# Performance work log

Hardware: AMD Instinct MI355X
Metric: run time of the kernel (lower is better)

Reference implementation:

```python
import jax, jax.numpy as jnp
import numpy as np

PALACE_N = 64   # base palace mask size
PALACE_BLOCK = 8  # 8 palaces of 8 positions each


def _palace_base():
    # base 64x64 mask: 1.0 within a palace (8x8 diagonal blocks), 0.5 across palaces
    pid = jnp.arange(PALACE_N) // PALACE_BLOCK
    intra = pid[:, None] == pid[None, :]
    return jnp.where(intra, 1.0, 0.5).astype(jnp.float32)


def _get_mask(T, inter_palace_weight):
    # tile base mask by index modulo 64 (matches mask[i % 64, j % 64])
    base = _palace_base()
    ii = jnp.arange(T) % PALACE_N
    base_T = base[ii[:, None], ii[None, :]]            # [T, T]
    intra = (base_T == 1.0).astype(jnp.float32)
    inter = (base_T < 1.0).astype(jnp.float32)
    return intra + jax.nn.sigmoid(inter_palace_weight) * inter


def setup_inputs() -> dict:
    key = jax.random.key(0)
    ks = jax.random.split(key, 5)
    B, T, D = 4, 2048, 1024
    x = jax.random.normal(ks[0], (B, T, D), dtype=jnp.float32)
    s = 1.0 / np.sqrt(D)
    Wq = jax.random.normal(ks[1], (D, D), dtype=jnp.float32) * s
    Wk = jax.random.normal(ks[2], (D, D), dtype=jnp.float32) * s
    Wv = jax.random.normal(ks[3], (D, D), dtype=jnp.float32) * s
    inter_palace_weight = jnp.float32(0.1)
    return {"x": x, "Wq": Wq, "Wk": Wk, "Wv": Wv,
            "inter_palace_weight": inter_palace_weight}


def reference(x, Wq, Wk, Wv, inter_palace_weight):
    B, T, D = x.shape
    H = 16
    hd = D // H
    scale = hd ** -0.5
    pmask = _get_mask(T, inter_palace_weight)          # [T, T]
    # torch Linear: x @ W.T
    q = (x @ Wq.T).reshape(B, T, H, hd)
    k = (x @ Wk.T).reshape(B, T, H, hd)
    v = (x @ Wv.T).reshape(B, T, H, hd)
    attn = jnp.einsum('bqhd,bkhd->bhqk', q, k) * scale
    attn = attn * pmask[None, None, :, :]
    attn = jax.nn.softmax(attn, axis=-1)
    attn = jnp.nan_to_num(attn, nan=0.0)
    out = jnp.einsum('bhqk,bkhd->bqhd', attn, v)
    return out.reshape(B, T, D)
```

## Files before the change

kernel.cpp:

```cpp
#include <hip/hip_runtime.h>

typedef unsigned short u16;
typedef unsigned int u32;
typedef short bf16x8 __attribute__((ext_vector_type(8)));
typedef short bf16x4 __attribute__((ext_vector_type(4)));
typedef float f32x4 __attribute__((ext_vector_type(4)));
typedef u32 u32x2 __attribute__((ext_vector_type(2)));

#define AS_GLOBAL __attribute__((address_space(1)))
#define AS_LDS __attribute__((address_space(3)))

#if defined(__HIP_DEVICE_COMPILE__)
#define MFMA16(a, b, c) __builtin_amdgcn_mfma_f32_16x16x16bf16_1k(a, b, c, 0, 0, 0)
#else
#define MFMA16(a, b, c) (c)
#endif

__device__ __forceinline__ void async16(const void* g, void* l) {
  __builtin_amdgcn_global_load_lds((const AS_GLOBAL u32*)g, (AS_LDS u32*)l, 16, 0, 0);
}

__device__ __forceinline__ u16 f2bf(float f) {
  u32 u = __builtin_bit_cast(u32, f);
  u += 0x7FFFu + ((u >> 16) & 1u);
  return (u16)(u >> 16);
}

__device__ __forceinline__ u32 pk2bf(float lo, float hi) {
  return __builtin_amdgcn_perm(__builtin_bit_cast(u32, hi),
                               __builtin_bit_cast(u32, lo), 0x07060302u);
}

__device__ __forceinline__ float fexp2(float x) {
#if __has_builtin(__builtin_amdgcn_exp2f)
  return __builtin_amdgcn_exp2f(x);
#else
  return exp2f(x);
#endif
}

__global__ __launch_bounds__(256) void cvt_all(const float* __restrict__ x,
                                               const float* __restrict__ wq,
                                               const float* __restrict__ wk,
                                               const float* __restrict__ wv,
                                               u16* __restrict__ xb,
                                               u16* __restrict__ wb) {
  const int blk = blockIdx.x;
  const float* src;
  u16* dst;
  int i;
  if (blk < 8192) {
    src = x; dst = xb; i = blk * 256 + threadIdx.x;
  } else if (blk < 9216) {
    src = wq; dst = wb; i = (blk - 8192) * 256 + threadIdx.x;
  } else if (blk < 10240) {
    src = wk; dst = wb + 1048576; i = (blk - 9216) * 256 + threadIdx.x;
  } else {
    src = wv; dst = wb + 2097152; i = (blk - 10240) * 256 + threadIdx.x;
  }
  float4 f = reinterpret_cast<const float4*>(src)[i];
  ushort4 o;
  o.x = f2bf(f.x); o.y = f2bf(f.y); o.z = f2bf(f.z); o.w = f2bf(f.w);
  reinterpret_cast<ushort4*>(dst)[i] = o;
}

__global__ __launch_bounds__(256, 3) void qkv_gemm(const u16* __restrict__ X,
                                                   const u16* __restrict__ W,
                                                   u16* __restrict__ O) {
  const int z = blockIdx.z;
  const u16* Wz = W + (size_t)z * (1024 * 1024);
  u16* Oz = O + (size_t)z * (8192 * 1024);

  __shared__ __align__(16) u16 As[2][128 * 32];
  __shared__ __align__(16) u16 Bs[2][128 * 32];

  const int t = threadIdx.x;
  const int lane = t & 63, w = t >> 6, quad = lane >> 4, lq = lane & 15;
  const int wm = (w >> 1) * 64, wn = (w & 1) * 64;
  const size_t m0 = (size_t)blockIdx.x * 128;
  const int n0 = blockIdx.y * 128;
  const int srow = t >> 2, sseg = (t & 3) * 8;

  f32x4 acc[4][4];
#pragma unroll
  for (int i = 0; i < 4; ++i)
#pragma unroll
    for (int j = 0; j < 4; ++j) acc[i][j] = f32x4{0.f, 0.f, 0.f, 0.f};

  const u16* ga = X + (m0 + srow) * 1024 + sseg;
  const u16* gb = Wz + (size_t)(n0 + srow) * 1024 + sseg;

  async16(ga, &As[0][srow * 32 + sseg]);
  async16(ga + 64 * 1024, &As[0][(64 + srow) * 32 + sseg]);
  async16(gb, &Bs[0][srow * 32 + sseg]);
  async16(gb + 64 * 1024, &Bs[0][(64 + srow) * 32 + sseg]);

  for (int kt = 0; kt < 32; ++kt) {
    const int cur = kt & 1;
    __syncthreads();
    if (kt < 31) {
      const int k1 = (kt + 1) * 32;
      async16(ga + k1, &As[cur ^ 1][srow * 32 + sseg]);
      async16(ga + 64 * 1024 + k1, &As[cur ^ 1][(64 + srow) * 32 + sseg]);
      async16(gb + k1, &Bs[cur ^ 1][srow * 32 + sseg]);
      async16(gb + 64 * 1024 + k1, &Bs[cur ^ 1][(64 + srow) * 32 + sseg]);
    }
    bf16x8 af[4], bfr[4];
#pragma unroll
    for (int i = 0; i < 4; ++i)
      af[i] = *reinterpret_cast<const bf16x8*>(&As[cur][(wm + i * 16 + lq) * 32 + quad * 8]);
#pragma unroll
    for (int j = 0; j < 4; ++j)
      bfr[j] = *reinterpret_cast<const bf16x8*>(&Bs[cur][(wn + j * 16 + lq) * 32 + quad * 8]);
#pragma unroll
    for (int i = 0; i < 4; ++i)
#pragma unroll
      for (int j = 0; j < 4; ++j)
        acc[i][j] = __builtin_amdgcn_mfma_f32_16x16x32_bf16(af[i], bfr[j], acc[i][j], 0, 0, 0);
  }

#pragma unroll
  for (int i = 0; i < 4; ++i) {
#pragma unroll
    for (int j = 0; j < 4; ++j) {
      const int n = n0 + wn + j * 16 + lq;
      const int hh = n >> 6, d = n & 63;
#pragma unroll
      for (int r = 0; r < 4; ++r) {
        const size_t m = m0 + wm + i * 16 + quad * 4 + r;
        const size_t bb = m >> 11, tt = m & 2047;
        if (z != 2)
          Oz[((bb * 16 + hh) * 2048 + tt) * 64 + d] = f2bf(acc[i][j][r]);
        else
          Oz[((bb * 16 + hh) * 64 + d) * 2048 + tt] = f2bf(acc[i][j][r]);
      }
    }
  }
}

__global__ __launch_bounds__(256, 2) void palace_attn(const u16* __restrict__ Q,
                                                      const u16* __restrict__ K,
                                                      const u16* __restrict__ Vt,
                                                      float* __restrict__ out,
                                                      const float* __restrict__ wptr) {
  const int bh = blockIdx.x, qt = blockIdx.y;
  const int h = bh & 15, b = bh >> 4;
  const size_t base = (size_t)bh * (2048 * 64);

  __shared__ __align__(16) u16 Ks[2][64 * 64];
  __shared__ __align__(16) u16 Vs[2][64 * 64];

  const int t = threadIdx.x;
  const int w = t >> 6, lane = t & 63, quad = lane >> 4, lq = lane & 15;
  const int q1 = quad >> 1, q0 = quad & 1, x7 = lq & 7;
  const float sig = 1.f / (1.f + __expf(-wptr[0]));
  const float Ci = 0.125f * 1.44269504f;
  const float Co = Ci * sig;
  const float MC = 14.4269504f;

  const float Cd = ((lq >> 3) == q1) ? Ci : Co;

  bf16x8 qf[4][2];
#pragma unroll
  for (int qg = 0; qg < 4; ++qg)
#pragma unroll
    for (int kc = 0; kc < 2; ++kc)
      qf[qg][kc] = *reinterpret_cast<const bf16x8*>(
          Q + base + (size_t)(qt * 256 + w * 64 + qg * 16 + lq) * 64 + kc * 32 + quad * 8);

  int ko[2], vo[2];
#pragma unroll
  for (int r = 0; r < 2; ++r) {
    const int slot = r * 256 + t;
    const int row = slot >> 3;
    const int cl = (slot & 7) ^ (row & 7);
    ko[r] = row * 64 + cl * 8;
    vo[r] = row * 2048 + cl * 8;
  }

  f32x4 O[4][4];
  float lsum[4] = {0.f, 0.f, 0.f, 0.f};
#pragma unroll
  for (int qg = 0; qg < 4; ++qg)
#pragma unroll
    for (int dg = 0; dg < 4; ++dg) O[qg][dg] = f32x4{0.f, 0.f, 0.f, 0.f};

  {
    const u16* kgp = K + base;
    const u16* vgp = Vt + base;
    async16(kgp + ko[0], &Ks[0][(w * 64) * 8]);
    async16(kgp + ko[1], &Ks[0][(256 + w * 64) * 8]);
    async16(vgp + vo[0], &Vs[0][(w * 64) * 8]);
    async16(vgp + vo[1], &Vs[0][(256 + w * 64) * 8]);
  }

  for (int kt = 0; kt < 32; ++kt) {
    const int cur = kt & 1;
    __syncthreads();
    if (kt < 31) {
      const u16* kgp = K + base + (size_t)(kt + 1) * 4096;
      const u16* vgp = Vt + base + (size_t)(kt + 1) * 64;
      const int nb = cur ^ 1;
      async16(kgp + ko[0], &Ks[nb][(w * 64) * 8]);
      async16(kgp + ko[1], &Ks[nb][(256 + w * 64) * 8]);
      async16(vgp + vo[0], &Vs[nb][(w * 64) * 8]);
      async16(vgp + vo[1], &Vs[nb][(256 + w * 64) * 8]);
    }

#pragma unroll
    for (int kg = 0; kg < 4; ++kg) {
      const bf16x8 kf0 = *reinterpret_cast<const bf16x8*>(
          &Ks[cur][((kg * 16 + lq) * 8 + (quad ^ x7)) * 8]);
      const bf16x8 kf1 = *reinterpret_cast<const bf16x8*>(
          &Ks[cur][((kg * 16 + lq) * 8 + ((4 + quad) ^ x7)) * 8]);
      f32x4 s[4];
#pragma unroll
      for (int qg = 0; qg < 4; ++qg) {
        f32x4 z = {0.f, 0.f, 0.f, 0.f};
        z = __builtin_amdgcn_mfma_f32_16x16x32_bf16(kf0, qf[qg][0], z, 0, 0, 0);
        s[qg] = __builtin_amdgcn_mfma_f32_16x16x32_bf16(kf1, qf[qg][1], z, 0, 0, 0);
      }

      const int c16 = (2 * kg + q1) ^ x7;
      bf16x4 vb[4];
#pragma unroll
      for (int dg = 0; dg < 4; ++dg)
        vb[dg] = *reinterpret_cast<const bf16x4*>(
            &Vs[cur][(dg * 16 + lq) * 64 + c16 * 8 + q0 * 4]);

#pragma unroll
      for (int qg = 0; qg < 4; ++qg) {
        const float cf = (kg == qg) ? Cd : Co;
        float p0 = fexp2(__builtin_fmaf(s[qg][0], cf, -MC));
        float p1 = fexp2(__builtin_fmaf(s[qg][1], cf, -MC));
        float p2 = fexp2(__builtin_fmaf(s[qg][2], cf, -MC));
        float p3 = fexp2(__builtin_fmaf(s[qg][3], cf, -MC));
        lsum[qg] += (p0 + p1) + (p2 + p3);
        u32x2 pk;
        pk.x = pk2bf(p0, p1);
        pk.y = pk2bf(p2, p3);
        const bf16x4 pa = __builtin_bit_cast(bf16x4, pk);
#pragma unroll
        for (int dg = 0; dg < 4; ++dg)
          O[qg][dg] = MFMA16(pa, vb[dg], O[qg][dg]);
      }
    }
  }

  float inv[4];
#pragma unroll
  for (int qg = 0; qg < 4; ++qg) {
    float l = lsum[qg];
    l += __shfl_xor(l, 16, 64);
    l += __shfl_xor(l, 32, 64);
    inv[qg] = 1.f / l;
  }

#pragma unroll
  for (int qg = 0; qg < 4; ++qg) {
#pragma unroll
    for (int r = 0; r < 4; ++r) {
      const float iv = __shfl(inv[qg], quad * 4 + r, 64);
      const size_t trow = (size_t)(qt * 256 + w * 64 + qg * 16 + quad * 4 + r);
      float* op = out + ((size_t)b * 2048 + trow) * 1024 + h * 64 + lq;
#pragma unroll
      for (int dg = 0; dg < 4; ++dg) op[dg * 16] = O[qg][dg][r] * iv;
    }
  }
}

extern "C" void kernel_launch(void* const* d_in, const int* in_sizes, int n_in,
                              void* d_out, int out_size, void* d_ws, size_t ws_size,
                              hipStream_t stream) {
  (void)in_sizes; (void)n_in; (void)out_size; (void)ws_size;
  const float* x = (const float*)d_in[0];
  const float* Wq = (const float*)d_in[1];
  const float* Wk = (const float*)d_in[2];
  const float* Wv = (const float*)d_in[3];
  const float* wip = (const float*)d_in[4];
  float* out = (float*)d_out;

  u16* xb = (u16*)d_ws;
  u16* wb = xb + 8388608;
  u16* qb = wb + 3145728;
  u16* kb = qb + 8388608;
  u16* vb = kb + 8388608;

  cvt_all<<<11264, 256, 0, stream>>>(x, Wq, Wk, Wv, xb, wb);
  qkv_gemm<<<dim3(64, 8, 3), 256, 0, stream>>>(xb, wb, qb);
  palace_attn<<<dim3(64, 8, 1), 256, 0, stream>>>(qb, kb, vb, out, wip);
}
```

Measured before the change: 259.5 us.

## Use 16x16x32 MFMA for PV, compute row sums via MFMA with ones

Restructures the key loop into two halves of 32 keys so each lane holds 8 probabilities. The PV product can then use the wider 16x16x32 bf16 MFMA instead of 16x16x16, with 8-wide V fragments. Row sums are accumulated by an extra MFMA against a ones vector, which removes the scalar adds and the cross-lane shuffles at the end. The K/V LDS swizzle and the palace mask coefficient table are reworked to match the new row mapping, at the cost of extra MFMAs for the sums.

```diff
diff --git a/kernel.cpp b/kernel.cpp
--- a/kernel.cpp
+++ b/kernel.cpp
@@ -3,18 +3,11 @@
 typedef unsigned short u16;
 typedef unsigned int u32;
 typedef short bf16x8 __attribute__((ext_vector_type(8)));
-typedef short bf16x4 __attribute__((ext_vector_type(4)));
 typedef float f32x4 __attribute__((ext_vector_type(4)));
-typedef u32 u32x2 __attribute__((ext_vector_type(2)));
+typedef u32 u32x4 __attribute__((ext_vector_type(4)));
 
 #define AS_GLOBAL __attribute__((address_space(1)))
 #define AS_LDS __attribute__((address_space(3)))
-
-#if defined(__HIP_DEVICE_COMPILE__)
-#define MFMA16(a, b, c) __builtin_amdgcn_mfma_f32_16x16x16bf16_1k(a, b, c, 0, 0, 0)
-#else
-#define MFMA16(a, b, c) (c)
-#endif
 
 __device__ __forceinline__ void async16(const void* g, void* l) {
   __builtin_amdgcn_global_load_lds((const AS_GLOBAL u32*)g, (AS_LDS u32*)l, 16, 0, 0);
@@ -152,13 +145,20 @@
 
   const int t = threadIdx.x;
   const int w = t >> 6, lane = t & 63, quad = lane >> 4, lq = lane & 15;
-  const int q1 = quad >> 1, q0 = quad & 1, x7 = lq & 7;
+  const int lq3 = lq >> 3;
+  const int swk = (lq & 3) | (((lq >> 2) & 1) << 2);
+  const int swv = (lq & 3) | (lq3 << 2);
   const float sig = 1.f / (1.f + __expf(-wptr[0]));
   const float Ci = 0.125f * 1.44269504f;
   const float Co = Ci * sig;
   const float MC = 14.4269504f;
 
-  const float Cd = ((lq >> 3) == q1) ? Ci : Co;
+  float cft[2][4];
+#pragma unroll
+  for (int half = 0; half < 2; ++half)
+#pragma unroll
+    for (int qg = 0; qg < 4; ++qg)
+      cft[half][qg] = (half * 4 + quad == qg * 2 + lq3) ? Ci : Co;
 
   bf16x8 qf[4][2];
 #pragma unroll
@@ -173,17 +173,23 @@
   for (int r = 0; r < 2; ++r) {
     const int slot = r * 256 + t;
     const int row = slot >> 3;
-    const int cl = (slot & 7) ^ (row & 7);
+    const int sr = (row & 3) | (((row >> 3) & 1) << 2);
+    const int cl = (slot & 7) ^ sr;
     ko[r] = row * 64 + cl * 8;
     vo[r] = row * 2048 + cl * 8;
   }
 
   f32x4 O[4][4];
-  float lsum[4] = {0.f, 0.f, 0.f, 0.f};
-#pragma unroll
-  for (int qg = 0; qg < 4; ++qg)
+  f32x4 Lacc[4];
+#pragma unroll
+  for (int qg = 0; qg < 4; ++qg) {
+    Lacc[qg] = f32x4{0.f, 0.f, 0.f, 0.f};
 #pragma unroll
     for (int dg = 0; dg < 4; ++dg) O[qg][dg] = f32x4{0.f, 0.f, 0.f, 0.f};
+  }
+
+  const short oneb = (short)0x3F80;
+  const bf16x8 ones8 = {oneb, oneb, oneb, oneb, oneb, oneb, oneb, oneb};
 
   {
     const u16* kgp = K + base;
@@ -208,59 +214,62 @@
     }
 
 #pragma unroll
-    for (int kg = 0; kg < 4; ++kg) {
-      const bf16x8 kf0 = *reinterpret_cast<const bf16x8*>(
-          &Ks[cur][((kg * 16 + lq) * 8 + (quad ^ x7)) * 8]);
-      const bf16x8 kf1 = *reinterpret_cast<const bf16x8*>(
-          &Ks[cur][((kg * 16 + lq) * 8 + ((4 + quad) ^ x7)) * 8]);
-      f32x4 s[4];
+    for (int half = 0; half < 2; ++half) {
+      const int rb = half * 32 + ((lq >> 2) << 3) + (lq & 3);
+      bf16x8 kf[2][2];
+#pragma unroll
+      for (int kg2 = 0; kg2 < 2; ++kg2) {
+        const int krow = rb + kg2 * 4;
+        kf[kg2][0] = *reinterpret_cast<const bf16x8*>(
+            &Ks[cur][krow * 64 + (quad ^ swk) * 8]);
+        kf[kg2][1] = *reinterpret_cast<const bf16x8*>(
+            &Ks[cur][krow * 64 + ((quad + 4) ^ swk) * 8]);
+      }
+
+      bf16x8 vbf[4];
+#pragma unroll
+      for (int dg = 0; dg < 4; ++dg)
+        vbf[dg] = *reinterpret_cast<const bf16x8*>(
+            &Vs[cur][(dg * 16 + lq) * 64 + ((half * 4 + quad) ^ swv) * 8]);
+
 #pragma unroll
       for (int qg = 0; qg < 4; ++qg) {
-        f32x4 z = {0.f, 0.f, 0.f, 0.f};
-        z = __builtin_amdgcn_mfma_f32_16x16x32_bf16(kf0, qf[qg][0], z, 0, 0, 0);
-        s[qg] = __builtin_amdgcn_mfma_f32_16x16x32_bf16(kf1, qf[qg][1], z, 0, 0, 0);
-      }
-
-      const int c16 = (2 * kg + q1) ^ x7;
-      bf16x4 vb[4];
-#pragma unroll
-      for (int dg = 0; dg < 4; ++dg)
-        vb[dg] = *reinterpret_cast<const bf16x4*>(
-            &Vs[cur][(dg * 16 + lq) * 64 + c16 * 8 + q0 * 4]);
-
-#pragma unroll
-      for (int qg = 0; qg < 4; ++qg) {
-        const float cf = (kg == qg) ? Cd : Co;
-        float p0 = fexp2(__builtin_fmaf(s[qg][0], cf, -MC));
-        float p1 = fexp2(__builtin_fmaf(s[qg][1], cf, -MC));
-        float p2 = fexp2(__builtin_fmaf(s[qg][2], cf, -MC));
-        float p3 = fexp2(__builtin_fmaf(s[qg][3], cf, -MC));
-        lsum[qg] += (p0 + p1) + (p2 + p3);
-        u32x2 pk;
+        f32x4 z0 = {0.f, 0.f, 0.f, 0.f}, z1 = {0.f, 0.f, 0.f, 0.f};
+        z0 = __builtin_amdgcn_mfma_f32_16x16x32_bf16(kf[0][0], qf[qg][0], z0, 0, 0, 0);
+        z0 = __builtin_amdgcn_mfma_f32_16x16x32_bf16(kf[0][1], qf[qg][1], z0, 0, 0, 0);
+        z1 = __builtin_amdgcn_mfma_f32_16x16x32_bf16(kf[1][0], qf[qg][0], z1, 0, 0, 0);
+        z1 = __builtin_amdgcn_mfma_f32_16x16x32_bf16(kf[1][1], qf[qg][1], z1, 0, 0, 0);
+
+        const float cf = cft[half][qg];
+        const float p0 = fexp2(__builtin_fmaf(z0[0], cf, -MC));
+        const float p1 = fexp2(__builtin_fmaf(z0[1], cf, -MC));
+        const float p2 = fexp2(__builtin_fmaf(z0[2], cf, -MC));
+        const float p3 = fexp2(__builtin_fmaf(z0[3], cf, -MC));
+        const float p4 = fexp2(__builtin_fmaf(z1[0], cf, -MC));
+        const float p5 = fexp2(__builtin_fmaf(z1[1], cf, -MC));
+        const float p6 = fexp2(__builtin_fmaf(z1[2], cf, -MC));
+        const float p7 = fexp2(__builtin_fmaf(z1[3], cf, -MC));
+
+        u32x4 pk;
         pk.x = pk2bf(p0, p1);
         pk.y = pk2bf(p2, p3);
-        const bf16x4 pa = __builtin_bit_cast(bf16x4, pk);
+        pk.z = pk2bf(p4, p5);
+        pk.w = pk2bf(p6, p7);
+        const bf16x8 pa = __builtin_bit_cast(bf16x8, pk);
+
+        Lacc[qg] = __builtin_amdgcn_mfma_f32_16x16x32_bf16(pa, ones8, Lacc[qg], 0, 0, 0);
 #pragma unroll
         for (int dg = 0; dg < 4; ++dg)
-          O[qg][dg] = MFMA16(pa, vb[dg], O[qg][dg]);
+          O[qg][dg] = __builtin_amdgcn_mfma_f32_16x16x32_bf16(pa, vbf[dg], O[qg][dg], 0, 0, 0);
       }
     }
   }
 
-  float inv[4];
 #pragma unroll
   for (int qg = 0; qg < 4; ++qg) {
-    float l = lsum[qg];
-    l += __shfl_xor(l, 16, 64);
-    l += __shfl_xor(l, 32, 64);
-    inv[qg] = 1.f / l;
-  }
-
-#pragma unroll
-  for (int qg = 0; qg < 4; ++qg) {
 #pragma unroll
     for (int r = 0; r < 4; ++r) {
-      const float iv = __shfl(inv[qg], quad * 4 + r, 64);
+      const float iv = 1.f / Lacc[qg][r];
       const size_t trow = (size_t)(qt * 256 + w * 64 + qg * 16 + quad * 4 + r);
       float* op = out + ((size_t)b * 2048 + trow) * 1024 + h * 64 + lq;
 #pragma unroll
```

After: 244.3 us. 5.9% less time.
